# Optimization experiments

Hardware: AMD Instinct MI355X
Metric: run time of the kernel (lower is better)

The kernel has to match this reference:

```python
import jax, jax.numpy as jnp
import numpy as np

SOBEL_X = jnp.array([[-1., 0., 1.], [-2., 0., 2.], [-1., 0., 1.]], dtype=jnp.float32).reshape(1, 1, 3, 3)
SOBEL_Y = jnp.array([[-1., -2., -1.], [0., 0., 0.], [1., 2., 1.]], dtype=jnp.float32).reshape(1, 1, 3, 3)


def setup_inputs() -> dict:
    key = jax.random.key(0)
    images = jax.random.uniform(key, (32, 3, 512, 512), dtype=jnp.float32)
    return {"images": images}


def _conv3x3(x, k):
    # x: [B,1,H,W], k: [1,1,3,3], SAME padding -> [B,1,H,W]
    return jax.lax.conv_general_dilated(
        x, k, window_strides=(1, 1), padding=((1, 1), (1, 1)),
        dimension_numbers=("NCHW", "OIHW", "NCHW"))


def reference(images):
    gray = jnp.mean(images, axis=1, keepdims=True)            # [B,1,H,W]
    edge_x = _conv3x3(gray, SOBEL_X)
    edge_y = _conv3x3(gray, SOBEL_Y)
    magnitude = jnp.sqrt(edge_x ** 2 + edge_y ** 2)           # [B,1,H,W]
    mx = jnp.max(magnitude, axis=(2, 3), keepdims=True)       # [B,1,1,1]
    edge_map = magnitude / (mx + 1e-6)
    return jnp.broadcast_to(edge_map, images.shape)           # [B,C,H,W]
```

## Files before the change

### kernel.cpp

```cpp
#include <hip/hip_runtime.h>
#include <hip/hip_bf16.h>

#define IMG_H 512
#define IMG_W 512
#define NB 32
#define NC 3
#define TILE_W 128
#define TILE_H 16
#define LDS_ROWS (TILE_H + 2)
#define LDS_F4_W 34
#define LDS_F_W  (LDS_F4_W * 4)
#define PLANE_F4 65536

__global__ __launch_bounds__(256) void sobel_mag_kernel(
    const float* __restrict__ in, float* __restrict__ out,
    unsigned int* __restrict__ maxbuf)
{
    __shared__ float4 g4[LDS_ROWS * LDS_F4_W];
    __shared__ float wmax[4];
    float* g = (float*)g4;

    const int b   = blockIdx.z;
    const int tx0 = blockIdx.x * TILE_W;
    const int ty0 = blockIdx.y * TILE_H;
    const int tid = threadIdx.x;

    const size_t HW = (size_t)IMG_H * IMG_W;
    const float4* base4 = (const float4*)(in + (size_t)b * NC * HW);

    const int tx0_4 = tx0 >> 2;
    #pragma unroll
    for (int k = 0; k < 3; ++k) {
        int idx = tid + k * 256;
        if (idx < LDS_ROWS * LDS_F4_W) {
            int row = idx / LDS_F4_W;
            int col = idx - row * LDS_F4_W;
            int gy  = ty0 + row - 1;
            int gx4 = tx0_4 + col - 1;
            float4 v = make_float4(0.f, 0.f, 0.f, 0.f);
            if (gy >= 0 && gy < IMG_H && gx4 >= 0 && gx4 < (IMG_W >> 2)) {
                const float4* p = base4 + (size_t)gy * (IMG_W >> 2) + gx4;
                float4 a = p[0];
                float4 c = p[PLANE_F4];
                float4 d = p[2 * PLANE_F4];
                v = make_float4((a.x + c.x + d.x) * (1.0f / 3.0f),
                                (a.y + c.y + d.y) * (1.0f / 3.0f),
                                (a.z + c.z + d.z) * (1.0f / 3.0f),
                                (a.w + c.w + d.w) * (1.0f / 3.0f));
            }
            g4[idx] = v;
        }
    }
    __syncthreads();

    float lmax = 0.0f;
    float* outb = out + (size_t)b * NC * HW;

    #pragma unroll
    for (int k = 0; k < 8; ++k) {
        int p  = tid + k * 256;
        int oy = p >> 7;
        int ox = p & 127;
        const float* r0 = g + (oy    ) * LDS_F_W + ox + 3;
        const float* r1 = g + (oy + 1) * LDS_F_W + ox + 3;
        const float* r2 = g + (oy + 2) * LDS_F_W + ox + 3;
        float a00 = r0[0], a01 = r0[1], a02 = r0[2];
        float a10 = r1[0],             a12 = r1[2];
        float a20 = r2[0], a21 = r2[1], a22 = r2[2];
        float sx = (a02 - a00) + 2.0f * (a12 - a10) + (a22 - a20);
        float sy = (a20 - a00) + 2.0f * (a21 - a01) + (a22 - a02);
        float mag = sqrtf(sx * sx + sy * sy);
        outb[(size_t)(ty0 + oy) * IMG_W + (tx0 + ox)] = mag;
        lmax = fmaxf(lmax, mag);
    }

    #pragma unroll
    for (int off = 32; off > 0; off >>= 1)
        lmax = fmaxf(lmax, __shfl_down(lmax, off, 64));
    if ((tid & 63) == 0) wmax[tid >> 6] = lmax;
    __syncthreads();
    if (tid == 0) {
        float m = fmaxf(fmaxf(wmax[0], wmax[1]), fmaxf(wmax[2], wmax[3]));
        atomicMax(&maxbuf[b], __float_as_uint(m));
    }
}

__global__ __launch_bounds__(256) void normalize_kernel(
    float* __restrict__ out, const unsigned int* __restrict__ maxbuf)
{
    const size_t HW = (size_t)IMG_H * IMG_W;
    const int b     = blockIdx.x >> 6;
    const int chunk = blockIdx.x & 63;

    const float mx  = __uint_as_float(maxbuf[b]);
    const float inv = 1.0f / (mx + 1e-6f);

    float4* c0 = (float4*)(out + (size_t)b * NC * HW);
    float4* c1 = (float4*)(out + ((size_t)b * NC + 1) * HW);
    float4* c2 = (float4*)(out + ((size_t)b * NC + 2) * HW);

    #pragma unroll
    for (int k = 0; k < 4; ++k) {
        int i = chunk * 1024 + k * 256 + threadIdx.x;
        float4 m = c0[i];
        float4 v = make_float4(m.x * inv, m.y * inv, m.z * inv, m.w * inv);
        c0[i] = v;
        c1[i] = v;
        c2[i] = v;
    }
}

extern "C" void kernel_launch(void* const* d_in, const int* in_sizes, int n_in,
                              void* d_out, int out_size, void* d_ws, size_t ws_size,
                              hipStream_t stream)
{
    const float* in  = (const float*)d_in[0];
    float*       out = (float*)d_out;
    unsigned int* maxbuf = (unsigned int*)d_ws;

    hipMemsetAsync(maxbuf, 0, NB * sizeof(unsigned int), stream);

    dim3 grid1(IMG_W / TILE_W, IMG_H / TILE_H, NB);
    sobel_mag_kernel<<<grid1, dim3(256, 1, 1), 0, stream>>>(in, out, maxbuf);

    normalize_kernel<<<dim3(NB * 64, 1, 1), dim3(256, 1, 1), 0, stream>>>(out, maxbuf);
}
```

Before: 215.2 us.

## Fuse sobel and normalize into one cooperative kernel with fp16 LDS staging

Merges the magnitude and normalization kernels into a single cooperative launch of 1024 blocks. Each block handles a full 16-row band, keeps the magnitudes in LDS as fp16, and after a grid-wide sync writes the normalized values to all three channels. This drops the write and re-read of the intermediate magnitude plane in global memory, plus one kernel launch. In exchange it adds a grid barrier and fp16 rounding of the magnitudes, which can introduce small precision error.

Measured after the change: 280.3 us. 30.3% more time.

```diff
diff --git a/kernel.cpp b/kernel.cpp
--- a/kernel.cpp
+++ b/kernel.cpp
@@ -1,112 +1,125 @@
 #include <hip/hip_runtime.h>
 #include <hip/hip_bf16.h>
+#include <hip/hip_fp16.h>
+#include <hip/hip_cooperative_groups.h>
 
-#define IMG_H 512
-#define IMG_W 512
-#define NB 32
-#define NC 3
-#define TILE_W 128
-#define TILE_H 16
+namespace cg = cooperative_groups;
+
+#define IMG      512
+#define ROW_F4   128
+#define PLANE_F4 65536
+#define NB       32
+#define NC       3
+#define TILE_W   128
+#define TILE_H   16
+#define NT       4
 #define LDS_ROWS (TILE_H + 2)
 #define LDS_F4_W 34
 #define LDS_F_W  (LDS_F4_W * 4)
-#define PLANE_F4 65536
 
-__global__ __launch_bounds__(256) void sobel_mag_kernel(
+__global__ __launch_bounds__(256, 4) void sobel_fused_kernel(
     const float* __restrict__ in, float* __restrict__ out,
     unsigned int* __restrict__ maxbuf)
 {
     __shared__ float4 g4[LDS_ROWS * LDS_F4_W];
-    __shared__ float wmax[4];
-    float* g = (float*)g4;
+    __shared__ short4 magl4[NT * 512];
+    __shared__ float  wred[4];
+    float*  g    = (float*)g4;
+    __half* magl = (__half*)magl4;
 
-    const int b   = blockIdx.z;
-    const int tx0 = blockIdx.x * TILE_W;
-    const int ty0 = blockIdx.y * TILE_H;
-    const int tid = threadIdx.x;
+    const int tid  = threadIdx.x;
+    const int b    = blockIdx.x >> 5;
+    const int band = blockIdx.x & 31;
+    const int ty0  = band * TILE_H;
 
-    const size_t HW = (size_t)IMG_H * IMG_W;
-    const float4* base4 = (const float4*)(in + (size_t)b * NC * HW);
-
-    const int tx0_4 = tx0 >> 2;
-    #pragma unroll
-    for (int k = 0; k < 3; ++k) {
-        int idx = tid + k * 256;
-        if (idx < LDS_ROWS * LDS_F4_W) {
-            int row = idx / LDS_F4_W;
-            int col = idx - row * LDS_F4_W;
-            int gy  = ty0 + row - 1;
-            int gx4 = tx0_4 + col - 1;
-            float4 v = make_float4(0.f, 0.f, 0.f, 0.f);
-            if (gy >= 0 && gy < IMG_H && gx4 >= 0 && gx4 < (IMG_W >> 2)) {
-                const float4* p = base4 + (size_t)gy * (IMG_W >> 2) + gx4;
-                float4 a = p[0];
-                float4 c = p[PLANE_F4];
-                float4 d = p[2 * PLANE_F4];
-                v = make_float4((a.x + c.x + d.x) * (1.0f / 3.0f),
-                                (a.y + c.y + d.y) * (1.0f / 3.0f),
-                                (a.z + c.z + d.z) * (1.0f / 3.0f),
-                                (a.w + c.w + d.w) * (1.0f / 3.0f));
-            }
-            g4[idx] = v;
-        }
-    }
-    __syncthreads();
+    const float4* base4 = (const float4*)in + (size_t)b * NC * PLANE_F4;
 
     float lmax = 0.0f;
-    float* outb = out + (size_t)b * NC * HW;
 
-    #pragma unroll
-    for (int k = 0; k < 8; ++k) {
-        int p  = tid + k * 256;
-        int oy = p >> 7;
-        int ox = p & 127;
-        const float* r0 = g + (oy    ) * LDS_F_W + ox + 3;
-        const float* r1 = g + (oy + 1) * LDS_F_W + ox + 3;
-        const float* r2 = g + (oy + 2) * LDS_F_W + ox + 3;
-        float a00 = r0[0], a01 = r0[1], a02 = r0[2];
-        float a10 = r1[0],             a12 = r1[2];
-        float a20 = r2[0], a21 = r2[1], a22 = r2[2];
-        float sx = (a02 - a00) + 2.0f * (a12 - a10) + (a22 - a20);
-        float sy = (a20 - a00) + 2.0f * (a21 - a01) + (a22 - a02);
-        float mag = sqrtf(sx * sx + sy * sy);
-        outb[(size_t)(ty0 + oy) * IMG_W + (tx0 + ox)] = mag;
-        lmax = fmaxf(lmax, mag);
+    for (int t = 0; t < NT; ++t) {
+        const int tx0   = t * TILE_W;
+        const int tx0_4 = tx0 >> 2;
+
+        #pragma unroll
+        for (int k = 0; k < 3; ++k) {
+            int idx = tid + k * 256;
+            if (idx < LDS_ROWS * LDS_F4_W) {
+                int row = idx / LDS_F4_W;
+                int col = idx - row * LDS_F4_W;
+                int gy  = ty0 + row - 1;
+                int gx4 = tx0_4 + col - 1;
+                float4 v = make_float4(0.f, 0.f, 0.f, 0.f);
+                if (gy >= 0 && gy < IMG && gx4 >= 0 && gx4 < ROW_F4) {
+                    const float4* p = base4 + (size_t)gy * ROW_F4 + gx4;
+                    float4 a = p[0];
+                    float4 c = p[PLANE_F4];
+                    float4 d = p[2 * PLANE_F4];
+                    v = make_float4((a.x + c.x + d.x) * (1.0f / 3.0f),
+                                    (a.y + c.y + d.y) * (1.0f / 3.0f),
+                                    (a.z + c.z + d.z) * (1.0f / 3.0f),
+                                    (a.w + c.w + d.w) * (1.0f / 3.0f));
+                }
+                g4[idx] = v;
+            }
+        }
+        __syncthreads();
+
+        #pragma unroll
+        for (int kk = 0; kk < 8; ++kk) {
+            int p  = tid + kk * 256;
+            int oy = p >> 7;
+            int ox = p & 127;
+            const float* r0 = g + (oy    ) * LDS_F_W + ox + 3;
+            const float* r1 = g + (oy + 1) * LDS_F_W + ox + 3;
+            const float* r2 = g + (oy + 2) * LDS_F_W + ox + 3;
+            float a00 = r0[0], a01 = r0[1], a02 = r0[2];
+            float a10 = r1[0],             a12 = r1[2];
+            float a20 = r2[0], a21 = r2[1], a22 = r2[2];
+            float sx = (a02 - a00) + 2.0f * (a12 - a10) + (a22 - a20);
+            float sy = (a20 - a00) + 2.0f * (a21 - a01) + (a22 - a02);
+            float mag = sqrtf(sx * sx + sy * sy);
+            magl[t * 2048 + p] = __float2half(mag);
+            lmax = fmaxf(lmax, mag);
+        }
+        __syncthreads();
     }
 
     #pragma unroll
-    for (int off = 32; off > 0; off >>= 1)
+    for (int off = 32; off; off >>= 1)
         lmax = fmaxf(lmax, __shfl_down(lmax, off, 64));
-    if ((tid & 63) == 0) wmax[tid >> 6] = lmax;
+    if ((tid & 63) == 0) wred[tid >> 6] = lmax;
     __syncthreads();
     if (tid == 0) {
-        float m = fmaxf(fmaxf(wmax[0], wmax[1]), fmaxf(wmax[2], wmax[3]));
-        atomicMax(&maxbuf[b], __float_as_uint(m));
+        float mb = fmaxf(fmaxf(wred[0], wred[1]), fmaxf(wred[2], wred[3]));
+        atomicMax(&maxbuf[b], __float_as_uint(mb));
     }
-}
 
-__global__ __launch_bounds__(256) void normalize_kernel(
-    float* __restrict__ out, const unsigned int* __restrict__ maxbuf)
-{
-    const size_t HW = (size_t)IMG_H * IMG_W;
-    const int b     = blockIdx.x >> 6;
-    const int chunk = blockIdx.x & 63;
+    cg::this_grid().sync();
 
-    const float mx  = __uint_as_float(maxbuf[b]);
-    const float inv = 1.0f / (mx + 1e-6f);
+    if (tid == 0) wred[0] = __uint_as_float(atomicMax(&maxbuf[b], 0u));
+    __syncthreads();
+    const float inv = 1.0f / (wred[0] + 1e-6f);
 
-    float4* c0 = (float4*)(out + (size_t)b * NC * HW);
-    float4* c1 = (float4*)(out + ((size_t)b * NC + 1) * HW);
-    float4* c2 = (float4*)(out + ((size_t)b * NC + 2) * HW);
-
+    float4* o0 = (float4*)out + (size_t)b * NC * PLANE_F4;
     #pragma unroll
-    for (int k = 0; k < 4; ++k) {
-        int i = chunk * 1024 + k * 256 + threadIdx.x;
-        float4 m = c0[i];
-        float4 v = make_float4(m.x * inv, m.y * inv, m.z * inv, m.w * inv);
-        c0[i] = v;
-        c1[i] = v;
-        c2[i] = v;
+    for (int t = 0; t < NT; ++t) {
+        const int tx0_4 = t * (TILE_W / 4);
+        #pragma unroll
+        for (int k = 0; k < 2; ++k) {
+            int fi  = k * 256 + tid;
+            int row = fi >> 5;
+            int col = fi & 31;
+            short4 h = magl4[t * 512 + fi];
+            const __half* hp = (const __half*)&h;
+            float4 v = make_float4(__half2float(hp[0]) * inv,
+                                   __half2float(hp[1]) * inv,
+                                   __half2float(hp[2]) * inv,
+                                   __half2float(hp[3]) * inv);
+            size_t o = (size_t)(ty0 + row) * ROW_F4 + tx0_4 + col;
+            o0[o]                = v;
+            o0[o + PLANE_F4]     = v;
+            o0[o + 2 * PLANE_F4] = v;
+        }
     }
 }
 
@@ -114,14 +127,14 @@
                               void* d_out, int out_size, void* d_ws, size_t ws_size,
                               hipStream_t stream)
 {
-    const float* in  = (const float*)d_in[0];
-    float*       out = (float*)d_out;
+    const float*  in     = (const float*)d_in[0];
+    float*        out    = (float*)d_out;
     unsigned int* maxbuf = (unsigned int*)d_ws;
 
     hipMemsetAsync(maxbuf, 0, NB * sizeof(unsigned int), stream);
 
-    dim3 grid1(IMG_W / TILE_W, IMG_H / TILE_H, NB);
-    sobel_mag_kernel<<<grid1, dim3(256, 1, 1), 0, stream>>>(in, out, maxbuf);
-
-    normalize_kernel<<<dim3(NB * 64, 1, 1), dim3(256, 1, 1), 0, stream>>>(out, maxbuf);
+    void* args[3] = { (void*)&in, (void*)&out, (void*)&maxbuf };
+    hipLaunchCooperativeKernel((const void*)sobel_fused_kernel,
+                               dim3(NB * 32, 1, 1), dim3(256, 1, 1),
+                               args, 0, stream);
 }
```

## Stage gradient magnitudes as fp16 in workspace and normalize with nontemporal stores

Applied to the files above, without the earlier changes.

When the workspace is large enough, the Sobel pass writes magnitudes as packed fp16 into a scratch buffer, two pixels per thread, instead of fp32 into the output. The normalize pass then reads this half-size buffer and writes all three channels with nontemporal stores, instead of reading back the fp32 output. This cuts intermediate traffic and avoids read-after-write on the output array. The cost is fp16 rounding of magnitudes before normalization, a precision risk, and the fast path depends on ws_size, with the old fp32 path kept as fallback.

Measured after the change: 210.9 us. -2.0%, faster.

```diff
diff --git a/kernel.cpp b/kernel.cpp
--- a/kernel.cpp
+++ b/kernel.cpp
@@ -1,19 +1,25 @@
 #include <hip/hip_runtime.h>
 #include <hip/hip_bf16.h>
-
-#define IMG_H 512
-#define IMG_W 512
-#define NB 32
-#define NC 3
-#define TILE_W 128
-#define TILE_H 16
+#include <hip/hip_fp16.h>
+
+#define IMG      512
+#define ROW_F4   128
+#define PLANE_F4 65536
+#define HW       (IMG * IMG)
+#define NB       32
+#define NC       3
+#define TILE_W   128
+#define TILE_H   16
 #define LDS_ROWS (TILE_H + 2)
 #define LDS_F4_W 34
 #define LDS_F_W  (LDS_F4_W * 4)
-#define PLANE_F4 65536
-
-__global__ __launch_bounds__(256) void sobel_mag_kernel(
-    const float* __restrict__ in, float* __restrict__ out,
+#define MAG_BYTES ((size_t)NB * HW * 2)
+
+typedef float vf4 __attribute__((ext_vector_type(4)));
+
+
+__global__ __launch_bounds__(256) void sobel_mag_f16(
+    const float* __restrict__ in, unsigned int* __restrict__ mag,
     unsigned int* __restrict__ maxbuf)
 {
     __shared__ float4 g4[LDS_ROWS * LDS_F4_W];
@@ -25,10 +31,9 @@
     const int ty0 = blockIdx.y * TILE_H;
     const int tid = threadIdx.x;
 
-    const size_t HW = (size_t)IMG_H * IMG_W;
-    const float4* base4 = (const float4*)(in + (size_t)b * NC * HW);
-
+    const float4* base4 = (const float4*)in + (size_t)b * NC * PLANE_F4;
     const int tx0_4 = tx0 >> 2;
+
     #pragma unroll
     for (int k = 0; k < 3; ++k) {
         int idx = tid + k * 256;
@@ -38,8 +43,8 @@
             int gy  = ty0 + row - 1;
             int gx4 = tx0_4 + col - 1;
             float4 v = make_float4(0.f, 0.f, 0.f, 0.f);
-            if (gy >= 0 && gy < IMG_H && gx4 >= 0 && gx4 < (IMG_W >> 2)) {
-                const float4* p = base4 + (size_t)gy * (IMG_W >> 2) + gx4;
+            if (gy >= 0 && gy < IMG && gx4 >= 0 && gx4 < ROW_F4) {
+                const float4* p = base4 + (size_t)gy * ROW_F4 + gx4;
                 float4 a = p[0];
                 float4 c = p[PLANE_F4];
                 float4 d = p[2 * PLANE_F4];
@@ -54,11 +59,123 @@
     __syncthreads();
 
     float lmax = 0.0f;
+    unsigned int* magb = mag + (size_t)b * (HW / 2)
+                             + (size_t)ty0 * (IMG / 2) + (tx0 >> 1);
+
+    #pragma unroll
+    for (int kk = 0; kk < 4; ++kk) {
+        int pp  = tid + kk * 256;
+        int oy  = pp >> 6;
+        int oxp = pp & 63;
+        int ox  = oxp << 1;
+        const float* r0 = g + oy * LDS_F_W + ox + 3;
+        const float* r1 = r0 + LDS_F_W;
+        const float* r2 = r1 + LDS_F_W;
+        float a0 = r0[0], a1 = r0[1], a2 = r0[2], a3 = r0[3];
+        float b0 = r1[0], b1 = r1[1], b2 = r1[2], b3 = r1[3];
+        float c0 = r2[0], c1 = r2[1], c2 = r2[2], c3 = r2[3];
+
+        float sx0 = (a2 - a0) + 2.0f * (b2 - b0) + (c2 - c0);
+        float sy0 = (c0 - a0) + 2.0f * (c1 - a1) + (c2 - a2);
+        float m0  = sqrtf(sx0 * sx0 + sy0 * sy0);
+        float sx1 = (a3 - a1) + 2.0f * (b3 - b1) + (c3 - c1);
+        float sy1 = (c1 - a1) + 2.0f * (c2 - a2) + (c3 - a3);
+        float m1  = sqrtf(sx1 * sx1 + sy1 * sy1);
+
+        lmax = fmaxf(lmax, fmaxf(m0, m1));
+        union { __half h[2]; unsigned int u; } pk;
+        pk.h[0] = __float2half(m0);
+        pk.h[1] = __float2half(m1);
+        magb[oy * (IMG / 2) + oxp] = pk.u;
+    }
+
+    #pragma unroll
+    for (int off = 32; off; off >>= 1)
+        lmax = fmaxf(lmax, __shfl_down(lmax, off, 64));
+    if ((tid & 63) == 0) wmax[tid >> 6] = lmax;
+    __syncthreads();
+    if (tid == 0) {
+        float mb = fmaxf(fmaxf(wmax[0], wmax[1]), fmaxf(wmax[2], wmax[3]));
+        atomicMax(&maxbuf[b], __float_as_uint(mb));
+    }
+}
+
+__global__ __launch_bounds__(256) void normalize_f16(
+    const uint2* __restrict__ mag, float* __restrict__ out,
+    const unsigned int* __restrict__ maxbuf)
+{
+    const int t = blockIdx.x * 256 + threadIdx.x;
+    vf4* o4 = (vf4*)out;
+
+    uint2 v[4];
+    #pragma unroll
+    for (int k = 0; k < 4; ++k)
+        v[k] = mag[(size_t)t + (size_t)k * 524288];
+
+    #pragma unroll
+    for (int k = 0; k < 4; ++k) {
+        int j   = t + k * 524288;
+        int b   = j >> 16;
+        int hw4 = j & (PLANE_F4 - 1);
+        float inv = 1.0f / (__uint_as_float(maxbuf[b]) + 1e-6f);
+
+        union { uint2 u; __half h[4]; } m; m.u = v[k];
+        vf4 f = { __half2float(m.h[0]) * inv,
+                  __half2float(m.h[1]) * inv,
+                  __half2float(m.h[2]) * inv,
+                  __half2float(m.h[3]) * inv };
+        size_t base = (size_t)b * NC * PLANE_F4 + hw4;
+        __builtin_nontemporal_store(f, &o4[base]);
+        __builtin_nontemporal_store(f, &o4[base + PLANE_F4]);
+        __builtin_nontemporal_store(f, &o4[base + 2 * PLANE_F4]);
+    }
+}
+
+
+__global__ __launch_bounds__(256) void sobel_mag_f32(
+    const float* __restrict__ in, float* __restrict__ out,
+    unsigned int* __restrict__ maxbuf)
+{
+    __shared__ float4 g4[LDS_ROWS * LDS_F4_W];
+    __shared__ float wmax[4];
+    float* g = (float*)g4;
+
+    const int b   = blockIdx.z;
+    const int tx0 = blockIdx.x * TILE_W;
+    const int ty0 = blockIdx.y * TILE_H;
+    const int tid = threadIdx.x;
+
+    const float4* base4 = (const float4*)in + (size_t)b * NC * PLANE_F4;
+    const int tx0_4 = tx0 >> 2;
+    #pragma unroll
+    for (int k = 0; k < 3; ++k) {
+        int idx = tid + k * 256;
+        if (idx < LDS_ROWS * LDS_F4_W) {
+            int row = idx / LDS_F4_W;
+            int col = idx - row * LDS_F4_W;
+            int gy  = ty0 + row - 1;
+            int gx4 = tx0_4 + col - 1;
+            float4 v = make_float4(0.f, 0.f, 0.f, 0.f);
+            if (gy >= 0 && gy < IMG && gx4 >= 0 && gx4 < ROW_F4) {
+                const float4* p = base4 + (size_t)gy * ROW_F4 + gx4;
+                float4 a = p[0];
+                float4 c = p[PLANE_F4];
+                float4 d = p[2 * PLANE_F4];
+                v = make_float4((a.x + c.x + d.x) * (1.0f / 3.0f),
+                                (a.y + c.y + d.y) * (1.0f / 3.0f),
+                                (a.z + c.z + d.z) * (1.0f / 3.0f),
+                                (a.w + c.w + d.w) * (1.0f / 3.0f));
+            }
+            g4[idx] = v;
+        }
+    }
+    __syncthreads();
+
+    float lmax = 0.0f;
     float* outb = out + (size_t)b * NC * HW;
-
-    #pragma unroll
-    for (int k = 0; k < 8; ++k) {
-        int p  = tid + k * 256;
+    #pragma unroll
+    for (int kk = 0; kk < 8; ++kk) {
+        int p  = tid + kk * 256;
         int oy = p >> 7;
         int ox = p & 127;
         const float* r0 = g + (oy    ) * LDS_F_W + ox + 3;
@@ -70,43 +187,35 @@
         float sx = (a02 - a00) + 2.0f * (a12 - a10) + (a22 - a20);
         float sy = (a20 - a00) + 2.0f * (a21 - a01) + (a22 - a02);
         float mag = sqrtf(sx * sx + sy * sy);
-        outb[(size_t)(ty0 + oy) * IMG_W + (tx0 + ox)] = mag;
+        outb[(size_t)(ty0 + oy) * IMG + (tx0 + ox)] = mag;
         lmax = fmaxf(lmax, mag);
     }
-
-    #pragma unroll
-    for (int off = 32; off > 0; off >>= 1)
+    #pragma unroll
+    for (int off = 32; off; off >>= 1)
         lmax = fmaxf(lmax, __shfl_down(lmax, off, 64));
     if ((tid & 63) == 0) wmax[tid >> 6] = lmax;
     __syncthreads();
     if (tid == 0) {
-        float m = fmaxf(fmaxf(wmax[0], wmax[1]), fmaxf(wmax[2], wmax[3]));
-        atomicMax(&maxbuf[b], __float_as_uint(m));
-    }
-}
-
-__global__ __launch_bounds__(256) void normalize_kernel(
+        float mb = fmaxf(fmaxf(wmax[0], wmax[1]), fmaxf(wmax[2], wmax[3]));
+        atomicMax(&maxbuf[b], __float_as_uint(mb));
+    }
+}
+
+__global__ __launch_bounds__(256) void normalize_f32(
     float* __restrict__ out, const unsigned int* __restrict__ maxbuf)
 {
-    const size_t HW = (size_t)IMG_H * IMG_W;
     const int b     = blockIdx.x >> 6;
     const int chunk = blockIdx.x & 63;
-
-    const float mx  = __uint_as_float(maxbuf[b]);
-    const float inv = 1.0f / (mx + 1e-6f);
-
-    float4* c0 = (float4*)(out + (size_t)b * NC * HW);
-    float4* c1 = (float4*)(out + ((size_t)b * NC + 1) * HW);
-    float4* c2 = (float4*)(out + ((size_t)b * NC + 2) * HW);
-
+    const float inv = 1.0f / (__uint_as_float(maxbuf[b]) + 1e-6f);
+    float4* c0 = (float4*)out + (size_t)b * NC * PLANE_F4;
     #pragma unroll
     for (int k = 0; k < 4; ++k) {
         int i = chunk * 1024 + k * 256 + threadIdx.x;
         float4 m = c0[i];
         float4 v = make_float4(m.x * inv, m.y * inv, m.z * inv, m.w * inv);
         c0[i] = v;
-        c1[i] = v;
-        c2[i] = v;
+        c0[i + PLANE_F4] = v;
+        c0[i + 2 * PLANE_F4] = v;
     }
 }
 
@@ -116,12 +225,20 @@
 {
     const float* in  = (const float*)d_in[0];
     float*       out = (float*)d_out;
-    unsigned int* maxbuf = (unsigned int*)d_ws;
-
-    hipMemsetAsync(maxbuf, 0, NB * sizeof(unsigned int), stream);
-
-    dim3 grid1(IMG_W / TILE_W, IMG_H / TILE_H, NB);
-    sobel_mag_kernel<<<grid1, dim3(256, 1, 1), 0, stream>>>(in, out, maxbuf);
-
-    normalize_kernel<<<dim3(NB * 64, 1, 1), dim3(256, 1, 1), 0, stream>>>(out, maxbuf);
-}
+
+    if (ws_size >= MAG_BYTES + 128) {
+        unsigned int* mag    = (unsigned int*)d_ws;
+        unsigned int* maxbuf = (unsigned int*)((char*)d_ws + MAG_BYTES);
+        (void)hipMemsetAsync(maxbuf, 0, NB * sizeof(unsigned int), stream);
+        dim3 grid1(IMG / TILE_W, IMG / TILE_H, NB);
+        sobel_mag_f16<<<grid1, dim3(256), 0, stream>>>(in, mag, maxbuf);
+        normalize_f16<<<dim3(2048), dim3(256), 0, stream>>>(
+            (const uint2*)mag, out, maxbuf);
+    } else {
+        unsigned int* maxbuf = (unsigned int*)d_ws;
+        (void)hipMemsetAsync(maxbuf, 0, NB * sizeof(unsigned int), stream);
+        dim3 grid1(IMG / TILE_W, IMG / TILE_H, NB);
+        sobel_mag_f32<<<grid1, dim3(256), 0, stream>>>(in, out, maxbuf);
+        normalize_f32<<<dim3(NB * 64), dim3(256), 0, stream>>>(out, maxbuf);
+    }
+}
```
